# Performance work log

Measured on AMD Instinct MI355X. Metric: run time of the kernel, lower is better.

Reference implementation:

```python
import jax, jax.numpy as jnp
import numpy as np

N_EMBED = 1024
N_HEAD = 16
HEAD_DIM = N_EMBED // N_HEAD
N_CONTEXT = 2048
MASKED_BIAS = -10000.0


def setup_inputs() -> dict:
    key = jax.random.key(0)
    k1, k2, k3 = jax.random.split(key, 3)
    hidden_states = jax.random.normal(k1, (4, 2048, N_EMBED), dtype=jnp.float32)
    w_attn = jax.random.normal(k2, (N_EMBED, 3 * N_EMBED), dtype=jnp.float32) * 0.02
    b_attn = jnp.zeros((3 * N_EMBED,), dtype=jnp.float32)
    w_proj = jax.random.normal(k3, (N_EMBED, N_EMBED), dtype=jnp.float32) * 0.02
    b_proj = jnp.zeros((N_EMBED,), dtype=jnp.float32)
    return {"hidden_states": hidden_states, "w_attn": w_attn, "b_attn": b_attn,
            "w_proj": w_proj, "b_proj": b_proj}


def reference(hidden_states, w_attn, b_attn, w_proj, b_proj):
    B, S, E = hidden_states.shape
    # c_attn: Conv1D (x @ W + b)
    qkv = hidden_states @ w_attn + b_attn  # [B,S,3E]
    q, k, v = jnp.split(qkv, 3, axis=-1)
    # split heads -> [B,H,S,D]
    def split_heads(x):
        return x.reshape(B, S, N_HEAD, HEAD_DIM).transpose(0, 2, 1, 3)
    q = split_heads(q)
    k = split_heads(k)  # torch permutes key to [B,H,D,S]; we keep [B,H,S,D] and einsum
    v = split_heads(v)
    # attention scores scaled by sqrt(head_dim) (v.size(-1) == HEAD_DIM)
    w = jnp.einsum('bhqd,bhkd->bhqk', q, k) / jnp.float32(HEAD_DIM) ** 0.5
    causal = jnp.tril(jnp.ones((S, S), dtype=bool))  # bias buffer slice
    w = jnp.where(causal[None, None], w, jnp.asarray(MASKED_BIAS, w.dtype))
    w = jax.nn.softmax(w, axis=-1)  # dropout p=0 -> identity
    out = jnp.einsum('bhqk,bhkd->bhqd', w, v)  # [B,H,S,D]
    # merge heads
    out = out.transpose(0, 2, 1, 3).reshape(B, S, E)
    out = out @ w_proj + b_proj
    # key returned in torch layout [B,H,D,S]
    return out, k.transpose(0, 1, 3, 2), v
```

## Files before the change

### kernel.cpp

```cpp
#include <hip/hip_runtime.h>
#include <hip/hip_bf16.h>


typedef __attribute__((ext_vector_type(8))) short bfx8;
typedef __attribute__((ext_vector_type(4))) short bfx4;
typedef __attribute__((ext_vector_type(4))) float fx4;

#define MFMA(a, b, c) __builtin_amdgcn_mfma_f32_16x16x32_bf16(a, b, c, 0, 0, 0)

#define S_CTX 2048
#define NE 1024
#define NH 16
#define HD 64

#define QSCALE 0.18033688011112042f

__device__ __forceinline__ short f2bf(float f) {
  unsigned u = __float_as_uint(f);
  unsigned r = u + 0x7fffu + ((u >> 16) & 1u);
  return (short)(r >> 16);
}

__device__ __forceinline__ unsigned pkbf(float a, float b) {
  union {
    __hip_bfloat162 h;
    unsigned u;
  } c;
  c.h = __float22bfloat162_rn(make_float2(a, b));
  return c.u;
}

__device__ __forceinline__ void gload16(const void* g, void* l) {
  __builtin_amdgcn_global_load_lds(
      (const __attribute__((address_space(1))) unsigned int*)g,
      (__attribute__((address_space(3))) unsigned int*)l, 16, 0, 0);
}

__global__ __launch_bounds__(256) void convert_bf16_kernel(const float* __restrict__ in,
                                                           short* __restrict__ out) {
  size_t i = (size_t)blockIdx.x * 256 + threadIdx.x;
  fx4 v = *(const fx4*)(in + i * 4);
  bfx4 o;
#pragma unroll
  for (int j = 0; j < 4; ++j) o[j] = f2bf(v[j]);
  *(bfx4*)(out + i * 4) = o;
}

__global__ __launch_bounds__(256) void transpose_conv_kernel(const float* __restrict__ in,
                                                             short* __restrict__ out,
                                                             int R, int C) {
  __shared__ float tile[32][33];
  int tx = threadIdx.x, ty = threadIdx.y;
  int c0 = blockIdx.x * 32, r0 = blockIdx.y * 32;
#pragma unroll
  for (int i = 0; i < 4; ++i)
    tile[ty + i * 8][tx] = in[(size_t)(r0 + ty + i * 8) * C + c0 + tx];
  __syncthreads();
#pragma unroll
  for (int i = 0; i < 4; ++i)
    out[(size_t)(c0 + ty + i * 8) * R + r0 + tx] = f2bf(tile[tx][ty + i * 8]);
}

__device__ __forceinline__ void gemm128_mainloop(const short* __restrict__ A,
                                                 const short* __restrict__ B,
                                                 const int K, const int m0, const int n0,
                                                 short* As, short* Bs, fx4 acc[4][4]) {
  const int t = threadIdx.x;
  const int lane = t & 63, w = t >> 6;
  const int g = lane >> 4, li = lane & 15;
  const int wr = w >> 1, wc = w & 1;
  const int bsw = ((lane & 7) ^ (lane >> 3)) * 8;
  const int rowl = w * 8 + (lane >> 3);

  for (int k0 = 0; k0 < K; k0 += 64) {
#pragma unroll
    for (int i = 0; i < 4; ++i) {
      const int row = i * 32 + rowl;
      gload16(A + (size_t)(m0 + row) * K + k0 + bsw, (char*)As + i * 4096 + w * 1024);
      gload16(B + (size_t)(n0 + row) * K + k0 + bsw, (char*)Bs + i * 4096 + w * 1024);
    }
    __syncthreads();
#pragma unroll
    for (int ks = 0; ks < 2; ++ks) {
      bfx8 af[4], bf[4];
#pragma unroll
      for (int m = 0; m < 4; ++m) {
        const int R = wr * 64 + m * 16 + li;
        af[m] = *(const bfx8*)((const char*)As + R * 128 + (((ks * 4 + g) ^ (li & 7)) << 4));
      }
#pragma unroll
      for (int n = 0; n < 4; ++n) {
        const int R = wc * 64 + n * 16 + li;
        bf[n] = *(const bfx8*)((const char*)Bs + R * 128 + (((ks * 4 + g) ^ (li & 7)) << 4));
      }
#pragma unroll
      for (int m = 0; m < 4; ++m)
#pragma unroll
        for (int n = 0; n < 4; ++n)
          acc[m][n] = MFMA(af[m], bf[n], acc[m][n]);
    }
    __syncthreads();
  }
}

__global__ __launch_bounds__(256) void gemm_qkv_kernel(const short* __restrict__ X,
                                                       const short* __restrict__ WT,
                                                       const float* __restrict__ bias,
                                                       short* __restrict__ qbf,
                                                       short* __restrict__ kbf,
                                                       short* __restrict__ vT,
                                                       float* __restrict__ kT,
                                                       float* __restrict__ vout) {
  __shared__ short As[128 * 64];
  __shared__ short Bs[128 * 64];
  fx4 acc[4][4];
  const fx4 z = {0.f, 0.f, 0.f, 0.f};
#pragma unroll
  for (int m = 0; m < 4; ++m)
#pragma unroll
    for (int n = 0; n < 4; ++n) acc[m][n] = z;
  const int m0 = blockIdx.x * 128, n0 = blockIdx.y * 128;
  gemm128_mainloop(X, WT, 1024, m0, n0, As, Bs, acc);

  const int lane = threadIdx.x & 63, w = threadIdx.x >> 6;
  const int g = lane >> 4, li = lane & 15;
  const int wr = w >> 1, wc = w & 1;
  const int sec = n0 >> 10;
#pragma unroll
  for (int mf = 0; mf < 4; ++mf) {
#pragma unroll
    for (int nf = 0; nf < 4; ++nf) {
      const int mrow = m0 + wr * 64 + mf * 16 + g * 4;
      const int ncol = n0 + wc * 64 + nf * 16 + li;
      const float bv = bias[ncol];
      fx4 vv;
#pragma unroll
      for (int jj = 0; jj < 4; ++jj) vv[jj] = acc[mf][nf][jj] + bv;
      const int b = mrow >> 11, s = mrow & 2047;
      const int e = ncol & 1023, h = e >> 6, d = e & 63;
      const size_t bidx = ((size_t)((b * 16 + h) * 2048 + s)) * 64 + d;
      if (sec == 0) {
#pragma unroll
        for (int jj = 0; jj < 4; ++jj) qbf[bidx + (size_t)jj * 64] = f2bf(vv[jj] * QSCALE);
      } else if (sec == 1) {
#pragma unroll
        for (int jj = 0; jj < 4; ++jj) kbf[bidx + (size_t)jj * 64] = f2bf(vv[jj]);
        const size_t tb = ((size_t)((b * 16 + h) * 64 + d)) * 2048 + s;
        *(fx4*)(kT + tb) = vv;
      } else {
#pragma unroll
        for (int jj = 0; jj < 4; ++jj) vout[bidx + (size_t)jj * 64] = vv[jj];
        const size_t tb = ((size_t)((b * 16 + h) * 64 + d)) * 2048 + s;
        bfx4 pv;
#pragma unroll
        for (int jj = 0; jj < 4; ++jj) pv[jj] = f2bf(vv[jj]);
        *(bfx4*)(vT + tb) = pv;
      }
    }
  }
}

__global__ __launch_bounds__(256) void gemm_proj_kernel(const short* __restrict__ X,
                                                        const short* __restrict__ WT,
                                                        const float* __restrict__ bias,
                                                        float* __restrict__ out) {
  __shared__ short As[128 * 64];
  __shared__ short Bs[128 * 64];
  fx4 acc[4][4];
  const fx4 z = {0.f, 0.f, 0.f, 0.f};
#pragma unroll
  for (int m = 0; m < 4; ++m)
#pragma unroll
    for (int n = 0; n < 4; ++n) acc[m][n] = z;
  const int m0 = blockIdx.x * 128, n0 = blockIdx.y * 128;
  gemm128_mainloop(X, WT, 1024, m0, n0, As, Bs, acc);

  const int lane = threadIdx.x & 63, w = threadIdx.x >> 6;
  const int g = lane >> 4, li = lane & 15;
  const int wr = w >> 1, wc = w & 1;
#pragma unroll
  for (int mf = 0; mf < 4; ++mf) {
#pragma unroll
    for (int nf = 0; nf < 4; ++nf) {
      const int mrow = m0 + wr * 64 + mf * 16 + g * 4;
      const int ncol = n0 + wc * 64 + nf * 16 + li;
      const float bv = bias[ncol];
#pragma unroll
      for (int jj = 0; jj < 4; ++jj)
        out[(size_t)(mrow + jj) * 1024 + ncol] = acc[mf][nf][jj] + bv;
    }
  }
}

#define KSW(base, row, byte) ((char*)(base) + (row) * 128 + ((byte) ^ (((row) & 7) << 4)))

#define SOFTMAX_TILE(stv, accv, mrun, lrun, pAv, qm, diag)                    \
  {                                                                          \
    if (diag) {                                                              \
      const int qg = (qm) + li;                                              \
      _Pragma("unroll") for (int kt = 0; kt < 4; ++kt)                       \
          _Pragma("unroll") for (int jj = 0; jj < 4; ++jj) if (              \
              k0 + kt * 16 + g * 4 + jj > qg) stv[kt][jj] = -1e30f;          \
    }                                                                        \
    float pm = stv[0][0];                                                    \
    _Pragma("unroll") for (int kt = 0; kt < 4; ++kt)                         \
        _Pragma("unroll") for (int jj = 0; jj < 4; ++jj) pm =                \
            fmaxf(pm, stv[kt][jj]);                                          \
    if (!__all(pm <= (mrun) + 6.0f)) {                                       \
      pm = fmaxf(pm, __shfl_xor(pm, 16));                                    \
      pm = fmaxf(pm, __shfl_xor(pm, 32));                                    \
      const float mn = fmaxf((mrun), pm);                                    \
      const float rf = __builtin_amdgcn_exp2f((mrun) - mn);                  \
      (lrun) *= rf;                                                          \
      fx4 rfv;                                                               \
      _Pragma("unroll") for (int jj = 0; jj < 4; ++jj) rfv[jj] =             \
          __shfl(rf, g * 4 + jj);                                            \
      _Pragma("unroll") for (int dt = 0; dt < 4; ++dt) accv[dt] *= rfv;      \
      (mrun) = mn;                                                           \
    }                                                                        \
    union {                                                                  \
      bfx8 v;                                                                \
      unsigned u[4];                                                         \
    } pk_[2];                                                                \
    float ls = 0.f;                                                          \
    _Pragma("unroll") for (int kt = 0; kt < 4; ++kt) {                       \
      const float p0 = __builtin_amdgcn_exp2f(stv[kt][0] - (mrun));          \
      const float p1 = __builtin_amdgcn_exp2f(stv[kt][1] - (mrun));          \
      const float p2 = __builtin_amdgcn_exp2f(stv[kt][2] - (mrun));          \
      const float p3 = __builtin_amdgcn_exp2f(stv[kt][3] - (mrun));          \
      ls += (p0 + p1) + (p2 + p3);                                           \
      pk_[kt >> 1].u[(kt & 1) * 2 + 0] = pkbf(p0, p1);                       \
      pk_[kt >> 1].u[(kt & 1) * 2 + 1] = pkbf(p2, p3);                       \
    }                                                                        \
    ls += __shfl_xor(ls, 16);                                                \
    ls += __shfl_xor(ls, 32);                                                \
    (lrun) += ls;                                                            \
    pAv[0] = pk_[0].v;                                                       \
    pAv[1] = pk_[1].v;                                                       \
  }

__global__ __launch_bounds__(256, 4) void attn_kernel(const short* __restrict__ Q,
                                                      const short* __restrict__ Kc,
                                                      const short* __restrict__ VT,
                                                      short* __restrict__ O) {
  __shared__ short Ks[2][64 * 64];
  __shared__ short Vs[2][64 * 64];

  const int bh = blockIdx.x & 63;
  const int c = blockIdx.x >> 6;

  const int t = threadIdx.x;
  const int w = t >> 6;
  const int lane = t & 63;
  const int g = lane >> 4, li = lane & 15;

  const size_t hoff = (size_t)bh * (S_CTX * HD);
  const short* Qh = Q + hoff;
  const char* Khc = (const char*)(Kc + hoff);
  const char* Vhc = (const char*)(VT + hoff);

  const int lr = lane >> 3;
  const int bsw = ((lane & 7) ^ lr) * 16;
  const int rb0 = w * 16;

  const int qm0 = 64 * c + 16 * w;
  const int qm1 = 64 * (31 - c) + 16 * w;
  bfx8 qf0[2], qf1[2];
  qf0[0] = *(const bfx8*)(Qh + (size_t)(qm0 + li) * HD + g * 8);
  qf0[1] = *(const bfx8*)(Qh + (size_t)(qm0 + li) * HD + 32 + g * 8);
  qf1[0] = *(const bfx8*)(Qh + (size_t)(qm1 + li) * HD + g * 8);
  qf1[1] = *(const bfx8*)(Qh + (size_t)(qm1 + li) * HD + 32 + g * 8);

  fx4 acc0[4], acc1[4];
  const fx4 z = {0.f, 0.f, 0.f, 0.f};
#pragma unroll
  for (int dt = 0; dt < 4; ++dt) {
    acc0[dt] = z;
    acc1[dt] = z;
  }
  float m0 = -1e30f, l0 = 0.f, m1 = -1e30f, l1 = 0.f;

  const int tmax = 31 - c;

#define STAGE_TILE(k0s, buf)                                                        \
  {                                                                                 \
    _Pragma("unroll") for (int i = 0; i < 2; ++i) {                                 \
      const int rb = rb0 + i * 8;                                                   \
      const int row = rb + lr;                                                      \
      gload16(Khc + (size_t)((k0s) + row) * 128 + bsw, (char*)Ks[buf] + rb * 128);  \
      gload16(Vhc + (size_t)row * (S_CTX * 2) + (size_t)(k0s) * 2 + bsw,            \
              (char*)Vs[buf] + rb * 128);                                           \
    }                                                                               \
  }

  STAGE_TILE(0, 0);
  __syncthreads();

  for (int tt = 0; tt <= tmax; ++tt) {
    const int cur = tt & 1;
    const int k0 = tt * 64;
    if (tt < tmax) STAGE_TILE(k0 + 64, cur ^ 1);
    const bool act0 = (tt <= c);

    bfx8 pA0[2], pA1[2];
    {
      fx4 st[4] = {z, z, z, z};
#pragma unroll
      for (int h = 0; h < 2; ++h) {
        bfx8 kfh[4];
#pragma unroll
        for (int kt = 0; kt < 4; ++kt)
          kfh[kt] = *(const bfx8*)KSW(Ks[cur], kt * 16 + li, h * 64 + g * 16);
#pragma unroll
        for (int kt = 0; kt < 4; ++kt) st[kt] = MFMA(kfh[kt], qf1[h], st[kt]);
      }
      SOFTMAX_TILE(st, acc1, m1, l1, pA1, qm1, tt == tmax);
    }
    if (act0) {
      fx4 st[4] = {z, z, z, z};
#pragma unroll
      for (int h = 0; h < 2; ++h) {
        bfx8 kfh[4];
#pragma unroll
        for (int kt = 0; kt < 4; ++kt)
          kfh[kt] = *(const bfx8*)KSW(Ks[cur], kt * 16 + li, h * 64 + g * 16);
#pragma unroll
        for (int kt = 0; kt < 4; ++kt) st[kt] = MFMA(kfh[kt], qf0[h], st[kt]);
      }
      SOFTMAX_TILE(st, acc0, m0, l0, pA0, qm0, tt == c);
    }
#pragma unroll
    for (int kc = 0; kc < 2; ++kc) {
      bfx8 vfc[4];
#pragma unroll
      for (int dt = 0; dt < 4; ++dt) {
        const int row = dt * 16 + li;
        const bfx4 a = *(const bfx4*)KSW(Vs[cur], row, kc * 64 + g * 8);
        const bfx4 b = *(const bfx4*)KSW(Vs[cur], row, kc * 64 + 32 + g * 8);
        bfx8 vv;
#pragma unroll
        for (int j = 0; j < 4; ++j) {
          vv[j] = a[j];
          vv[j + 4] = b[j];
        }
        vfc[dt] = vv;
      }
#pragma unroll
      for (int dt = 0; dt < 4; ++dt) acc1[dt] = MFMA(pA1[kc], vfc[dt], acc1[dt]);
      if (act0) {
#pragma unroll
        for (int dt = 0; dt < 4; ++dt) acc0[dt] = MFMA(pA0[kc], vfc[dt], acc0[dt]);
      }
    }
    __syncthreads();
  }

  const int b = bh >> 4, h = bh & 15;
#pragma unroll
  for (int mf = 0; mf < 2; ++mf) {
    const int qm = mf ? qm1 : qm0;
    const float lr_ = mf ? l1 : l0;
    fx4 lv;
#pragma unroll
    for (int jj = 0; jj < 4; ++jj)
      lv[jj] = __builtin_amdgcn_rcpf(__shfl(lr_, g * 4 + jj));
#pragma unroll
    for (int dt = 0; dt < 4; ++dt)
#pragma unroll
      for (int jj = 0; jj < 4; ++jj) {
        const int s = qm + g * 4 + jj;
        const fx4 av = mf ? acc1[dt] : acc0[dt];
        O[((size_t)(b * S_CTX + s)) * NE + h * HD + dt * 16 + li] =
            f2bf(av[jj] * lv[jj]);
      }
  }
}

extern "C" void kernel_launch(void* const* d_in, const int* in_sizes, int n_in,
                              void* d_out, int out_size, void* d_ws, size_t ws_size,
                              hipStream_t stream) {
  const float* hs = (const float*)d_in[0];
  const float* w_attn = (const float*)d_in[1];
  const float* b_attn = (const float*)d_in[2];
  const float* w_proj = (const float*)d_in[3];
  const float* b_proj = (const float*)d_in[4];

  float* out = (float*)d_out;
  float* kT_out = out + 8388608;
  float* v_out = out + 2 * 8388608;

  char* ws = (char*)d_ws;
  short* xbf = (short*)ws;
  short* waT = (short*)(ws + 16777216);
  short* vTb = (short*)(ws + 23068672);
  short* qbf = (short*)(ws + 39845888);
  short* kbf = (short*)(ws + 56623104);
  short* wpT = (short*)(ws + 73400320);

  convert_bf16_kernel<<<8192, 256, 0, stream>>>(hs, xbf);
  transpose_conv_kernel<<<dim3(96, 32), dim3(32, 8), 0, stream>>>(w_attn, waT, 1024, 3072);
  transpose_conv_kernel<<<dim3(32, 32), dim3(32, 8), 0, stream>>>(w_proj, wpT, 1024, 1024);
  gemm_qkv_kernel<<<dim3(64, 24), 256, 0, stream>>>(xbf, waT, b_attn, qbf, kbf, vTb,
                                                    kT_out, v_out);
  attn_kernel<<<1024, 256, 0, stream>>>(qbf, kbf, vTb, xbf );
  gemm_proj_kernel<<<dim3(64, 8), 256, 0, stream>>>(xbf, wpT, b_proj, out);
}
```

Measured before the change: 178.0 us.

## Triple-buffer GEMM mainloop with async global-to-LDS prefetch two stages ahead

Replaces the single-buffered K=64 GEMM mainloop with a three-stage ring of K=32 LDS buffers. Tiles are issued two iterations ahead, and a vmcnt wait plus one barrier per step replaces the load-sync-compute-sync pattern. The aim is to hide global load latency behind MFMA work and drop one barrier per step. In exchange each step does half the MFMA work, adds more LDS (24KB vs 16KB) and relies on hand-written waitcnt/barrier ordering, which could create a race if the vmcnt count is wrong.

```diff
diff --git a/kernel.cpp b/kernel.cpp
--- a/kernel.cpp
+++ b/kernel.cpp
@@ -64,43 +64,63 @@
 __device__ __forceinline__ void gemm128_mainloop(const short* __restrict__ A,
                                                  const short* __restrict__ B,
                                                  const int K, const int m0, const int n0,
-                                                 short* As, short* Bs, fx4 acc[4][4]) {
+                                                 short* As3, short* Bs3, fx4 acc[4][4]) {
   const int t = threadIdx.x;
   const int lane = t & 63, w = t >> 6;
   const int g = lane >> 4, li = lane & 15;
   const int wr = w >> 1, wc = w & 1;
-  const int bsw = ((lane & 7) ^ (lane >> 3)) * 8;
-  const int rowl = w * 8 + (lane >> 3);
-
-  for (int k0 = 0; k0 < K; k0 += 64) {
-#pragma unroll
-    for (int i = 0; i < 4; ++i) {
-      const int row = i * 32 + rowl;
-      gload16(A + (size_t)(m0 + row) * K + k0 + bsw, (char*)As + i * 4096 + w * 1024);
-      gload16(B + (size_t)(n0 + row) * K + k0 + bsw, (char*)Bs + i * 4096 + w * 1024);
-    }
-    __syncthreads();
-#pragma unroll
-    for (int ks = 0; ks < 2; ++ks) {
-      bfx8 af[4], bf[4];
-#pragma unroll
-      for (int m = 0; m < 4; ++m) {
-        const int R = wr * 64 + m * 16 + li;
-        af[m] = *(const bfx8*)((const char*)As + R * 128 + (((ks * 4 + g) ^ (li & 7)) << 4));
-      }
-#pragma unroll
-      for (int n = 0; n < 4; ++n) {
-        const int R = wc * 64 + n * 16 + li;
-        bf[n] = *(const bfx8*)((const char*)Bs + R * 128 + (((ks * 4 + g) ^ (li & 7)) << 4));
-      }
-#pragma unroll
-      for (int m = 0; m < 4; ++m)
-#pragma unroll
-        for (int n = 0; n < 4; ++n)
-          acc[m][n] = MFMA(af[m], bf[n], acc[m][n]);
-    }
-    __syncthreads();
-  }
+  const int l2 = lane >> 2;
+  const int bsw = ((lane & 3) ^ (l2 & 3)) * 8;
+  const int NT = K >> 5;
+
+#define GSTG3(tt)                                                    \
+  {                                                                  \
+    const int kk = (tt) * 32;                                        \
+    const int bb = ((tt) % 3) * 8192;                                \
+    _Pragma("unroll") for (int j = 0; j < 2; ++j) {                  \
+      const int rowb = (j * 4 + w) * 16 + l2;                        \
+      gload16(A + (size_t)(m0 + rowb) * K + kk + bsw,                \
+              (char*)As3 + bb + (j * 4 + w) * 1024);                 \
+      gload16(B + (size_t)(n0 + rowb) * K + kk + bsw,                \
+              (char*)Bs3 + bb + (j * 4 + w) * 1024);                 \
+    }                                                                \
+  }
+
+  GSTG3(0);
+  GSTG3(1);
+  asm volatile("s_waitcnt vmcnt(4)" ::: "memory");
+  __builtin_amdgcn_sched_barrier(0);
+  asm volatile("s_barrier" ::: "memory");
+
+  for (int tt = 0; tt < NT; ++tt) {
+    if (tt + 2 < NT) GSTG3(tt + 2);
+    const char* Ab = (const char*)As3 + (tt % 3) * 8192;
+    const char* Bb = (const char*)Bs3 + (tt % 3) * 8192;
+    bfx8 af[4], bf[4];
+#pragma unroll
+    for (int m = 0; m < 4; ++m) {
+      const int R = wr * 64 + m * 16 + li;
+      af[m] = *(const bfx8*)(Ab + R * 64 + ((g ^ (li & 3)) << 4));
+    }
+#pragma unroll
+    for (int n = 0; n < 4; ++n) {
+      const int R = wc * 64 + n * 16 + li;
+      bf[n] = *(const bfx8*)(Bb + R * 64 + ((g ^ (li & 3)) << 4));
+    }
+#pragma unroll
+    for (int m = 0; m < 4; ++m)
+#pragma unroll
+      for (int n = 0; n < 4; ++n)
+        acc[m][n] = MFMA(af[m], bf[n], acc[m][n]);
+    if (tt + 2 < NT) {
+      asm volatile("s_waitcnt vmcnt(4)" ::: "memory");
+    } else {
+      asm volatile("s_waitcnt vmcnt(0)" ::: "memory");
+    }
+    __builtin_amdgcn_sched_barrier(0);
+    asm volatile("s_barrier" ::: "memory");
+  }
+#undef GSTG3
 }
 
 __global__ __launch_bounds__(256) void gemm_qkv_kernel(const short* __restrict__ X,
@@ -111,8 +131,8 @@
                                                        short* __restrict__ vT,
                                                        float* __restrict__ kT,
                                                        float* __restrict__ vout) {
-  __shared__ short As[128 * 64];
-  __shared__ short Bs[128 * 64];
+  __shared__ short As3[3 * 128 * 32];
+  __shared__ short Bs3[3 * 128 * 32];
   fx4 acc[4][4];
   const fx4 z = {0.f, 0.f, 0.f, 0.f};
 #pragma unroll
@@ -120,7 +140,7 @@
 #pragma unroll
     for (int n = 0; n < 4; ++n) acc[m][n] = z;
   const int m0 = blockIdx.x * 128, n0 = blockIdx.y * 128;
-  gemm128_mainloop(X, WT, 1024, m0, n0, As, Bs, acc);
+  gemm128_mainloop(X, WT, 1024, m0, n0, As3, Bs3, acc);
 
   const int lane = threadIdx.x & 63, w = threadIdx.x >> 6;
   const int g = lane >> 4, li = lane & 15;
@@ -164,8 +184,8 @@
                                                         const short* __restrict__ WT,
                                                         const float* __restrict__ bias,
                                                         float* __restrict__ out) {
-  __shared__ short As[128 * 64];
-  __shared__ short Bs[128 * 64];
+  __shared__ short As3[3 * 128 * 32];
+  __shared__ short Bs3[3 * 128 * 32];
   fx4 acc[4][4];
   const fx4 z = {0.f, 0.f, 0.f, 0.f};
 #pragma unroll
@@ -173,7 +193,7 @@
 #pragma unroll
     for (int n = 0; n < 4; ++n) acc[m][n] = z;
   const int m0 = blockIdx.x * 128, n0 = blockIdx.y * 128;
-  gemm128_mainloop(X, WT, 1024, m0, n0, As, Bs, acc);
+  gemm128_mainloop(X, WT, 1024, m0, n0, As3, Bs3, acc);
 
   const int lane = threadIdx.x & 63, w = threadIdx.x >> 6;
   const int g = lane >> 4, li = lane & 15;
```

New measurement: 186.3 us. +4.7%, slower.
